# Optimization experiments

Measured on AMD Instinct MI355X. Metric: run time of the kernel, lower is better.

## Reference

```python
import jax, jax.numpy as jnp
import numpy as np

# Module hyperparameters (from init_kwargs)
EPS = 1.0
EMBS_DIM = 300
C = 0.005
N_SAMPLES = 1_000_000

# d = 2*C*sqrt(embs_dim); alpha = eps/d; scale = 1/alpha
_SCALE = float(2.0 * C * np.sqrt(EMBS_DIM) / EPS)
# A = -scale * log(1 - 2*eps/sqrt(embs_dim))  (truncation bound)
_A = float(-_SCALE * np.log(1.0 - 2.0 * EPS / np.sqrt(EMBS_DIM)))


def setup_inputs() -> dict:
    key = jax.random.key(0)
    k1, k2, k3 = jax.random.split(key, 3)
    embs = jax.random.normal(k1, (128, 1024, EMBS_DIM), dtype=jnp.float32)
    # pre-sampled Rademacher signs: sign of a standard normal is +/-1 w.p. 1/2
    sgn = jax.random.normal(k2, (N_SAMPLES,), dtype=jnp.float32)
    # uniform(0,1] draws (avoid exact 0 so log is finite, as np.random.uniform excludes 1 not 0 but log(0)=-inf is rejected by the mask anyway)
    u = jax.random.uniform(k3, (N_SAMPLES,), dtype=jnp.float32, minval=1e-12, maxval=1.0)
    return {"embs": embs, "sgn": sgn, "u": u}


def reference(embs, sgn, u):
    # Laplace via inverse-CDF: r = mean - scale * sgn * log(U), mean = 0
    r = -_SCALE * jnp.sign(sgn) * jnp.log(u)  # [N_SAMPLES]
    # rejection: keep samples inside [-A, A]
    mask = (r >= -_A) & (r <= _A)
    # fixed-size truncation r_tr[:EMBS_DIM] without data-dependent shapes:
    # pos = rank among accepted samples; accepted samples with rank < EMBS_DIM
    # scatter into a buffer, everything else scatters into a dropped slot.
    pos = jnp.cumsum(mask.astype(jnp.int32)) - 1  # rank of each accepted sample
    target = jnp.where(mask & (pos < EMBS_DIM), pos, EMBS_DIM)
    buf = jnp.zeros(EMBS_DIM + 1, dtype=embs.dtype).at[target].set(r.astype(embs.dtype))
    noise = buf[:EMBS_DIM]  # first EMBS_DIM accepted samples
    # broadcast add over [..., EMBS_DIM]
    return embs + noise
```

## Files before the change

### kernel.cpp

```cpp
#include <hip/hip_runtime.h>
#include <math.h>

#define EMBS_DIM 300
#define SCAN_BLOCK 1024

__global__ __launch_bounds__(SCAN_BLOCK) void build_noise_kernel(
    const float* __restrict__ sgn, const float* __restrict__ u, int n,
    float* __restrict__ noise, float scale, float A)
{
    __shared__ int s_wave_tot[SCAN_BLOCK / 64];
    const int tid  = threadIdx.x;
    const int lane = tid & 63;
    const int wave = tid >> 6;
    const int nwaves = SCAN_BLOCK / 64;

    for (int j = tid; j < EMBS_DIM; j += SCAN_BLOCK) noise[j] = 0.0f;
    __syncthreads();

    int base = 0;
    for (int i0 = 0; i0 < n; i0 += SCAN_BLOCK) {
        const int i = i0 + tid;
        float r = 0.0f;
        int m = 0;
        if (i < n) {
            const float s  = sgn[i];
            const float sg = (s > 0.0f) ? 1.0f : ((s < 0.0f) ? -1.0f : 0.0f);
            r = (-scale * sg) * logf(u[i]);
            m = (r >= -A && r <= A) ? 1 : 0;
        }
        const unsigned long long bal = __ballot(m);
        if (lane == 0) s_wave_tot[wave] = __popcll(bal);
        __syncthreads();
        int woff = 0, tot = 0;
        #pragma unroll
        for (int w = 0; w < nwaves; ++w) {
            const int t = s_wave_tot[w];
            if (w < wave) woff += t;
            tot += t;
        }
        const int lpre = __popcll(bal & ((1ull << lane) - 1ull));
        const int pos  = base + woff + lpre;
        if (m && pos < EMBS_DIM) noise[pos] = r;
        base += tot;
        __syncthreads();
        if (base >= EMBS_DIM) break;
    }
}

__global__ __launch_bounds__(256) void add_noise_kernel(
    const float4* __restrict__ embs, const float4* __restrict__ noise4,
    float4* __restrict__ out, int total4)
{
    const int i = blockIdx.x * 256 + threadIdx.x;
    if (i >= total4) return;
    const int j = i % (EMBS_DIM / 4);
    const float4 e  = embs[i];
    const float4 nv = noise4[j];
    float4 o;
    o.x = e.x + nv.x;
    o.y = e.y + nv.y;
    o.z = e.z + nv.z;
    o.w = e.w + nv.w;
    out[i] = o;
}

extern "C" void kernel_launch(void* const* d_in, const int* in_sizes, int n_in,
                              void* d_out, int out_size, void* d_ws, size_t ws_size,
                              hipStream_t stream)
{
    const float* embs = (const float*)d_in[0];
    const float* sgn  = (const float*)d_in[1];
    const float* u    = (const float*)d_in[2];
    float* out   = (float*)d_out;
    float* noise = (float*)d_ws;

    const int n = in_sizes[1];

    const double scaled = 2.0 * 0.005 * sqrt(300.0) / 1.0;
    const double Ad     = -scaled * log(1.0 - 2.0 * 1.0 / sqrt(300.0));
    const float scale = (float)scaled;
    const float A     = (float)Ad;

    build_noise_kernel<<<1, SCAN_BLOCK, 0, stream>>>(sgn, u, n, noise, scale, A);

    const int total4 = out_size / 4;
    const int blocks = (total4 + 255) / 256;
    add_noise_kernel<<<blocks, 256, 0, stream>>>(
        (const float4*)embs, (const float4*)noise, (float4*)out, total4);
}
```

Before: 267.8 us.

## Fuse noise construction into add kernel with per-block redundant scan

Result: slower. 278.7 us (+4.0%).

```diff
diff --git a/kernel.cpp b/kernel.cpp
--- a/kernel.cpp
+++ b/kernel.cpp
@@ -2,23 +2,27 @@
 #include <math.h>
 
 #define EMBS_DIM 300
-#define SCAN_BLOCK 1024
+#define TPB 1024
+#define NBLOCKS 512
 
-__global__ __launch_bounds__(SCAN_BLOCK) void build_noise_kernel(
-    const float* __restrict__ sgn, const float* __restrict__ u, int n,
-    float* __restrict__ noise, float scale, float A)
+__global__ __launch_bounds__(TPB) void fused_noise_add_kernel(
+    const float4* __restrict__ embs, const float* __restrict__ sgn,
+    const float* __restrict__ u, int n, float4* __restrict__ out,
+    int total4, float scale, float A)
 {
-    __shared__ int s_wave_tot[SCAN_BLOCK / 64];
+    __shared__ int s_wave_tot[TPB / 64];
+    __shared__ __align__(16) float s_noise[EMBS_DIM + 4];
+
     const int tid  = threadIdx.x;
     const int lane = tid & 63;
     const int wave = tid >> 6;
-    const int nwaves = SCAN_BLOCK / 64;
+    const int nwaves = TPB / 64;
 
-    for (int j = tid; j < EMBS_DIM; j += SCAN_BLOCK) noise[j] = 0.0f;
+    if (tid < EMBS_DIM + 4) s_noise[tid] = 0.0f;
     __syncthreads();
 
     int base = 0;
-    for (int i0 = 0; i0 < n; i0 += SCAN_BLOCK) {
+    for (int i0 = 0; i0 < n; i0 += TPB) {
         const int i = i0 + tid;
         float r = 0.0f;
         int m = 0;
@@ -40,28 +44,30 @@
         }
         const int lpre = __popcll(bal & ((1ull << lane) - 1ull));
         const int pos  = base + woff + lpre;
-        if (m && pos < EMBS_DIM) noise[pos] = r;
+        if (m && pos < EMBS_DIM) s_noise[pos] = r;
         base += tot;
         __syncthreads();
         if (base >= EMBS_DIM) break;
     }
-}
+    __syncthreads();
 
-__global__ __launch_bounds__(256) void add_noise_kernel(
-    const float4* __restrict__ embs, const float4* __restrict__ noise4,
-    float4* __restrict__ out, int total4)
-{
-    const int i = blockIdx.x * 256 + threadIdx.x;
-    if (i >= total4) return;
-    const int j = i % (EMBS_DIM / 4);
-    const float4 e  = embs[i];
-    const float4 nv = noise4[j];
-    float4 o;
-    o.x = e.x + nv.x;
-    o.y = e.y + nv.y;
-    o.z = e.z + nv.z;
-    o.w = e.w + nv.w;
-    out[i] = o;
+    const float4* noise4 = (const float4*)s_noise;
+    const int stride = gridDim.x * TPB;
+    const int jstep = stride % 75;
+    int i = blockIdx.x * TPB + tid;
+    int j = i % 75;
+    for (; i < total4; i += stride) {
+        const float4 e  = embs[i];
+        const float4 nv = noise4[j];
+        float4 o;
+        o.x = e.x + nv.x;
+        o.y = e.y + nv.y;
+        o.z = e.z + nv.z;
+        o.w = e.w + nv.w;
+        out[i] = o;
+        j += jstep;
+        if (j >= 75) j -= 75;
+    }
 }
 
 extern "C" void kernel_launch(void* const* d_in, const int* in_sizes, int n_in,
@@ -71,8 +77,7 @@
     const float* embs = (const float*)d_in[0];
     const float* sgn  = (const float*)d_in[1];
     const float* u    = (const float*)d_in[2];
-    float* out   = (float*)d_out;
-    float* noise = (float*)d_ws;
+    float* out = (float*)d_out;
 
     const int n = in_sizes[1];
 
@@ -81,10 +86,8 @@
     const float scale = (float)scaled;
     const float A     = (float)Ad;
 
-    build_noise_kernel<<<1, SCAN_BLOCK, 0, stream>>>(sgn, u, n, noise, scale, A);
+    const int total4 = out_size / 4;
 
-    const int total4 = out_size / 4;
-    const int blocks = (total4 + 255) / 256;
-    add_noise_kernel<<<blocks, 256, 0, stream>>>(
-        (const float4*)embs, (const float4*)noise, (float4*)out, total4);
+    fused_noise_add_kernel<<<NBLOCKS, TPB, 0, stream>>>(
+        (const float4*)embs, sgn, u, n, (float4*)out, total4, scale, A);
 }
```
